# Performance work log

Hardware: AMD Instinct MI355X
Metric: run time of the kernel (lower is better)

## Reference

```python
import jax, jax.numpy as jnp
import numpy as np

N, H, R, E = 100000, 128, 30, 600000
EPS = 1e-5  # BatchNorm1d default eps


def _rgcn_layer(h, src, dst, etype, W, root, bias):
    """PyG RGCNConv: out = h @ root + bias + sum_r scatter_mean_r(h[src] @ W[r]).
    Mean is per (dst, relation) edge count."""
    n = h.shape[0]
    r_count = W.shape[0]
    seg = dst * r_count + etype                      # combined (dst, rel) segment id
    deg = jax.ops.segment_sum(jnp.ones_like(etype, dtype=h.dtype), seg,
                              num_segments=n * r_count)
    norm = 1.0 / jnp.maximum(deg[seg], 1.0)          # (E,) per-edge mean weight

    def body(out, inp):
        Wr, r = inp
        xr = h @ Wr                                  # (N,H) relation-transformed feats
        contrib = jnp.where((etype == r)[:, None], xr[src] * norm[:, None], 0.0)
        return out + jax.ops.segment_sum(contrib, dst, num_segments=n), None

    out0 = h @ root + bias
    out, _ = jax.lax.scan(body, out0, (W, jnp.arange(r_count)))
    return out


def _bn_relu(h, gamma, beta):
    # BatchNorm1d in training mode: biased batch statistics over the node dim
    mu = h.mean(axis=0)
    var = h.var(axis=0)
    return jax.nn.relu((h - mu) * jax.lax.rsqrt(var + EPS) * gamma + beta)


def setup_inputs() -> dict:
    key = jax.random.key(0)
    ks = jax.random.split(key, 16)
    s = 1.0 / np.sqrt(H)
    return {
        "x": jnp.arange(N, dtype=jnp.int32),
        "edge_index": jax.random.randint(ks[0], (2, E), 0, N, dtype=jnp.int32),
        "edge_type": jax.random.randint(ks[1], (E,), 0, R, dtype=jnp.int32),
        "emb": jax.random.normal(ks[2], (N, H), jnp.float32) * s,
        "W1": jax.random.normal(ks[3], (R, H, H), jnp.float32) * s,
        "root1": jax.random.normal(ks[4], (H, H), jnp.float32) * s,
        "b1": jnp.zeros((H,), jnp.float32),
        "g1": jnp.ones((H,), jnp.float32),
        "be1": jnp.zeros((H,), jnp.float32),
        "W2": jax.random.normal(ks[5], (R, H, H), jnp.float32) * s,
        "root2": jax.random.normal(ks[6], (H, H), jnp.float32) * s,
        "b2": jnp.zeros((H,), jnp.float32),
        "g2": jnp.ones((H,), jnp.float32),
        "be2": jnp.zeros((H,), jnp.float32),
    }


def reference(x, edge_index, edge_type, emb, W1, root1, b1, g1, be1,
              W2, root2, b2, g2, be2):
    src, dst = edge_index[0], edge_index[1]
    h = emb[x]                                        # (N,H) embedding lookup
    h = _bn_relu(_rgcn_layer(h, src, dst, edge_type, W1, root1, b1), g1, be1)
    h = _bn_relu(_rgcn_layer(h, src, dst, edge_type, W2, root2, b2), g2, be2)
    return h  # dropout is identity (deterministic reference)
```

## Files before the change

kernel.cpp:

```cpp
#include <hip/hip_runtime.h>
#include <hip/hip_bf16.h>

#define NN 100000
#define HH 128
#define RR 30
#define NE 600000
#define TILE 64
#define CH 64
#define EPAD (NE + RR * TILE)
#define NCHMAX (EPAD / TILE)
#define NB_PS ((NN + 255) / 256)
#define NBLK_BN 784
#define RPB_BN 128
#define BN_EPS 1e-5f

typedef __bf16 v8bf __attribute__((ext_vector_type(8)));
typedef float  v4f  __attribute__((ext_vector_type(4)));
typedef unsigned int v4u __attribute__((ext_vector_type(4)));

static __device__ __forceinline__ unsigned short f2b(float f) {
    unsigned int u = __float_as_uint(f);
    unsigned int r = (u + 0x7FFF + ((u >> 16) & 1)) >> 16;
    return (unsigned short)r;
}

__global__ void k_hist(const int* __restrict__ dst, const int* __restrict__ et,
                       int* __restrict__ deg, int* __restrict__ cnt) {
    __shared__ int lh[RR];
    int t = threadIdx.x;
    if (t < RR) lh[t] = 0;
    __syncthreads();
    int i = blockIdx.x * blockDim.x + t;
    if (i < NE) {
        int d = dst[i], r = et[i];
        atomicAdd(&deg[d * RR + r], 1);
        atomicAdd(&lh[r], 1);
    }
    __syncthreads();
    if (t < RR && lh[t]) atomicAdd(&cnt[t], lh[t]);
}

__global__ void k_degsum(const int* __restrict__ deg, int* __restrict__ cnt_d) {
    int d = blockIdx.x * blockDim.x + threadIdx.x;
    if (d >= NN) return;
    int s = 0;
#pragma unroll
    for (int r = 0; r < RR; ++r) s += deg[(size_t)d * RR + r];
    cnt_d[d] = s;
}

__global__ void k_scan(const int* __restrict__ cnt, int* __restrict__ cursor,
                       int* __restrict__ totals,
                       int* __restrict__ src_s, int* __restrict__ dst_s,
                       float* __restrict__ norm_s, int* __restrict__ dpos_s,
                       int* __restrict__ chunk_rel, int need_dst) {
    __shared__ int off[RR + 1];
    if (threadIdx.x == 0) {
        int acc = 0;
        for (int r = 0; r < RR; ++r) {
            off[r] = acc;
            acc += (cnt[r] + TILE - 1) / TILE;
        }
        off[RR] = acc;
        totals[0] = acc * TILE;
    }
    __syncthreads();
    for (int r = 0; r < RR; ++r) {
        for (int c = off[r] + (int)threadIdx.x; c < off[r + 1]; c += blockDim.x)
            chunk_rel[c] = r;
        int begin = off[r] * TILE + cnt[r];
        int end   = off[r + 1] * TILE;
        for (int p = begin + (int)threadIdx.x; p < end; p += blockDim.x) {
            src_s[p] = 0; norm_s[p] = 0.f;
            dpos_s[p] = NE;
            if (need_dst) dst_s[p] = 0;
        }
    }
    if (threadIdx.x == 0)
        for (int r = 0; r < RR; ++r) cursor[r] = off[r] * TILE;
}

__global__ void k_psum1(const int* __restrict__ c, int* __restrict__ bsum) {
    __shared__ int sh[256];
    int i = blockIdx.x * 256 + threadIdx.x;
    sh[threadIdx.x] = (i < NN) ? c[i] : 0;
    __syncthreads();
    for (int s = 128; s > 0; s >>= 1) {
        if (threadIdx.x < s) sh[threadIdx.x] += sh[threadIdx.x + s];
        __syncthreads();
    }
    if (threadIdx.x == 0) bsum[blockIdx.x] = sh[0];
}

__global__ void k_psum2(int* __restrict__ bsum) {
    __shared__ int sh[512];
    int t = threadIdx.x;
    sh[t] = (t < NB_PS) ? bsum[t] : 0;
    __syncthreads();
    if (t == 0) {
        int acc = 0;
        for (int b = 0; b < NB_PS; ++b) { int v = sh[b]; sh[b] = acc; acc += v; }
    }
    __syncthreads();
    if (t < NB_PS) bsum[t] = sh[t];
}

__global__ void k_psum3(const int* __restrict__ c, const int* __restrict__ bscan,
                        int* __restrict__ off, int* __restrict__ cur) {
    __shared__ int sh[256];
    int t = threadIdx.x;
    int i = blockIdx.x * 256 + t;
    int v = (i < NN) ? c[i] : 0;
    sh[t] = v;
    __syncthreads();
    for (int s = 1; s < 256; s <<= 1) {
        int a = (t >= s) ? sh[t - s] : 0;
        __syncthreads();
        sh[t] += a;
        __syncthreads();
    }
    int excl = sh[t] - v + bscan[blockIdx.x];
    if (i < NN) { off[i] = excl; cur[i] = excl; }
    if (i == 0) off[NN] = NE;
}

__global__ void k_fillds2(const int* __restrict__ off, int* __restrict__ ds2) {
    int d = blockIdx.x * blockDim.x + threadIdx.x;
    if (d >= NN) return;
    int s = off[d], e = off[d + 1];
    for (int p = s; p < e; ++p) ds2[p] = d;
}

__global__ void k_scatter(const int* __restrict__ src, const int* __restrict__ dst,
                          const int* __restrict__ et, const int* __restrict__ deg,
                          int* __restrict__ cursor, int* __restrict__ cursor_dst,
                          int* __restrict__ src_s, int* __restrict__ dst_s,
                          float* __restrict__ norm_s, int* __restrict__ dpos_s,
                          int need_dst) {
    __shared__ int lh[RR];
    __shared__ int lbase[RR];
    int t = threadIdx.x;
    if (t < RR) lh[t] = 0;
    __syncthreads();
    int i = blockIdx.x * blockDim.x + t;
    int r = 0, d = 0, lrank = 0;
    bool valid = (i < NE);
    if (valid) {
        r = et[i]; d = dst[i];
        lrank = atomicAdd(&lh[r], 1);
    }
    __syncthreads();
    if (t < RR && lh[t]) lbase[t] = atomicAdd(&cursor[t], lh[t]);
    __syncthreads();
    if (valid) {
        int pos = lbase[r] + lrank;
        src_s[pos] = src[i];
        if (need_dst) dst_s[pos] = d;
        int dg = deg[d * RR + r];
        norm_s[pos] = 1.0f / (float)(dg > 1 ? dg : 1);
        dpos_s[pos] = atomicAdd(&cursor_dst[d], 1);
    }
}

__global__ void k_convW(const float* __restrict__ W, unsigned short* __restrict__ Wt,
                        int total) {
    int idx = blockIdx.x * blockDim.x + threadIdx.x;
    if (idx >= total) return;
    int m = idx / (HH * HH);
    int rem = idx % (HH * HH);
    int k = rem / HH, c = rem % HH;
    Wt[m * HH * HH + c * HH + k] = f2b(W[idx]);
}

__global__ void k_embed(const int* __restrict__ x, const float* __restrict__ emb,
                        unsigned short* __restrict__ hb) {
    int idx = blockIdx.x * blockDim.x + threadIdx.x;
    if (idx >= NN * HH) return;
    int i = idx / HH, j = idx % HH;
    hb[idx] = f2b(emb[x[i] * HH + j]);
}

__global__ __launch_bounds__(256) void k_rootgemm(const unsigned short* __restrict__ hb,
                                                  const unsigned short* __restrict__ rootT,
                                                  const float* __restrict__ bias,
                                                  float* __restrict__ tmp) {
    __shared__ __align__(16) unsigned short Xs[TILE][HH + 8];
    __shared__ __align__(16) unsigned short Ws[HH][HH + 8];
    int base = blockIdx.x * TILE;
    int t = threadIdx.x;

    {
        int l = t >> 2, lr = t & 3;
        int row = base + l;
        for (int i = 0; i < 4; ++i) {
            int g = lr + 4 * i;
            uint4 v = {0u, 0u, 0u, 0u};
            if (row < NN) v = *reinterpret_cast<const uint4*>(hb + (size_t)row * HH + g * 8);
            *reinterpret_cast<uint4*>(&Xs[l][g * 8]) = v;
        }
    }
    for (int i = 0; i < 8; ++i) {
        int idx = t + 256 * i;
        int row = idx >> 4, g = idx & 15;
        *reinterpret_cast<uint4*>(&Ws[row][g * 8]) =
            *reinterpret_cast<const uint4*>(rootT + row * HH + g * 8);
    }
    __syncthreads();

    int w = t >> 6, lane = t & 63;
    int lr16 = lane & 15, kg = lane >> 4;
    v4f acc[8];
    for (int n = 0; n < 8; ++n) acc[n] = (v4f){0.f, 0.f, 0.f, 0.f};
#pragma unroll
    for (int kk = 0; kk < 4; ++kk) {
        int k0 = kk * 32 + kg * 8;
        v8bf a = *reinterpret_cast<const v8bf*>(&Xs[w * 16 + lr16][k0]);
#pragma unroll
        for (int n = 0; n < 8; ++n) {
            v8bf b = *reinterpret_cast<const v8bf*>(&Ws[n * 16 + lr16][k0]);
            acc[n] = __builtin_amdgcn_mfma_f32_16x16x32_bf16(a, b, acc[n], 0, 0, 0);
        }
    }
#pragma unroll
    for (int n = 0; n < 8; ++n)
        for (int j = 0; j < 4; ++j) {
            int row = base + w * 16 + kg * 4 + j;
            int col = n * 16 + lr16;
            if (row < NN) tmp[(size_t)row * HH + col] = acc[n][j] + bias[col];
        }
}

__global__ __launch_bounds__(256) void k_edgegemm_x(const unsigned short* __restrict__ hb,
                                                    const unsigned short* __restrict__ Wt,
                                                    const int* __restrict__ src_s,
                                                    const int* __restrict__ chunk_rel,
                                                    const float* __restrict__ norm_s,
                                                    const int* __restrict__ dpos_s,
                                                    const int* __restrict__ totals,
                                                    unsigned short* __restrict__ xe) {
    int ebase = blockIdx.x * TILE;
    if (ebase >= totals[0]) return;
    __shared__ __align__(16) unsigned short Ws[HH][HH + 8];
    __shared__ __align__(16) unsigned short Xs[TILE][HH];
    int t = threadIdx.x;
    int rel = chunk_rel[blockIdx.x];

    const unsigned short* Wr = Wt + (size_t)rel * HH * HH;
    for (int i = 0; i < 8; ++i) {
        int idx = t + 256 * i;
        int row = idx >> 4, g = idx & 15;
        *reinterpret_cast<uint4*>(&Ws[row][g * 8]) =
            *reinterpret_cast<const uint4*>(Wr + row * HH + g * 8);
    }

    int w = t >> 6, lane = t & 63;
    int lr16 = lane & 15, kg = lane >> 4;
    int slot = w * 16 + lr16;
    int srow = src_s[ebase + slot];
    float nrm = norm_s[ebase + slot];

    v8bf xf[4];
    const unsigned short* hrow = hb + (size_t)srow * HH + kg * 8;
#pragma unroll
    for (int kk = 0; kk < 4; ++kk)
        xf[kk] = *reinterpret_cast<const v8bf*>(hrow + kk * 32);

    __syncthreads();

    int c = slot & 7;
#pragma unroll
    for (int n = 0; n < 8; ++n) {
        v4f acc = {0.f, 0.f, 0.f, 0.f};
#pragma unroll
        for (int kk = 0; kk < 4; ++kk) {
            v8bf wf = *reinterpret_cast<const v8bf*>(&Ws[n * 16 + lr16][kk * 32 + kg * 8]);
            acc = __builtin_amdgcn_mfma_f32_16x16x32_bf16(wf, xf[kk], acc, 0, 0, 0);
        }
        unsigned long long p =
            (unsigned long long)f2b(acc[0] * nrm)
          | ((unsigned long long)f2b(acc[1] * nrm) << 16)
          | ((unsigned long long)f2b(acc[2] * nrm) << 32)
          | ((unsigned long long)f2b(acc[3] * nrm) << 48);
        int a = n * 4 + kg;
        int sw = (((a >> 1) ^ c) << 1) | (a & 1);
        *reinterpret_cast<unsigned long long*>(&Xs[slot][sw * 4]) = p;
    }
    __syncthreads();
    {
        int l = t >> 2, lr = t & 3;
        size_t drow = (size_t)dpos_s[ebase + l];
        int cs = l & 7;
        unsigned short* orow = xe + drow * HH;
#pragma unroll
        for (int i = 0; i < 4; ++i) {
            int j = lr + 4 * i;
            v4u v = *reinterpret_cast<const v4u*>(&Xs[l][(j ^ cs) * 8]);
            __builtin_nontemporal_store(v, reinterpret_cast<v4u*>(orow + j * 8));
        }
    }
}

__global__ __launch_bounds__(256) void k_edgegemm_at(const unsigned short* __restrict__ hb,
                                                     const unsigned short* __restrict__ Wt,
                                                     const int* __restrict__ src_s,
                                                     const int* __restrict__ dst_s,
                                                     const int* __restrict__ chunk_rel,
                                                     const float* __restrict__ norm_s,
                                                     const int* __restrict__ totals,
                                                     float* __restrict__ tmp) {
    int ebase = blockIdx.x * TILE;
    if (ebase >= totals[0]) return;
    __shared__ __align__(16) unsigned short Xs[TILE][HH + 8];
    __shared__ __align__(16) unsigned short Ws[HH][HH + 8];
    __shared__ int   src_l[TILE];
    __shared__ int   dst_l[TILE];
    __shared__ float nrm_l[TILE];
    int t = threadIdx.x;
    if (t < TILE) {
        src_l[t] = src_s[ebase + t];
        dst_l[t] = dst_s[ebase + t];
        nrm_l[t] = norm_s[ebase + t];
    }
    int rel = chunk_rel[blockIdx.x];
    __syncthreads();
    {
        int l = t >> 2, lr = t & 3;
        int srow = src_l[l];
        for (int i = 0; i < 4; ++i) {
            int g = lr + 4 * i;
            *reinterpret_cast<uint4*>(&Xs[l][g * 8]) =
                *reinterpret_cast<const uint4*>(hb + (size_t)srow * HH + g * 8);
        }
    }
    const unsigned short* Wr = Wt + (size_t)rel * HH * HH;
    for (int i = 0; i < 8; ++i) {
        int idx = t + 256 * i;
        int row = idx >> 4, g = idx & 15;
        *reinterpret_cast<uint4*>(&Ws[row][g * 8]) =
            *reinterpret_cast<const uint4*>(Wr + row * HH + g * 8);
    }
    __syncthreads();
    int w = t >> 6, lane = t & 63;
    int lr16 = lane & 15, kg = lane >> 4;
    v4f acc[8];
    for (int n = 0; n < 8; ++n) acc[n] = (v4f){0.f, 0.f, 0.f, 0.f};
#pragma unroll
    for (int kk = 0; kk < 4; ++kk) {
        int k0 = kk * 32 + kg * 8;
        v8bf a = *reinterpret_cast<const v8bf*>(&Xs[w * 16 + lr16][k0]);
#pragma unroll
        for (int n = 0; n < 8; ++n) {
            v8bf b = *reinterpret_cast<const v8bf*>(&Ws[n * 16 + lr16][k0]);
            acc[n] = __builtin_amdgcn_mfma_f32_16x16x32_bf16(a, b, acc[n], 0, 0, 0);
        }
    }
#pragma unroll
    for (int n = 0; n < 8; ++n)
        for (int j = 0; j < 4; ++j) {
            int slot = w * 16 + kg * 4 + j;
            int col  = n * 16 + lr16;
            atomicAdd(&tmp[(size_t)dst_l[slot] * HH + col], acc[n][j] * nrm_l[slot]);
        }
}

__global__ __launch_bounds__(256) void k_aggseg(const unsigned int* __restrict__ xe32,
                                                const int* __restrict__ ds2,
                                                float* __restrict__ tmp) {
    int wid = (blockIdx.x * blockDim.x + threadIdx.x) >> 6;
    int lane = threadIdx.x & 63;
    if (wid >= NE / CH) return;
    int c0 = wid * CH;

    int dme = ds2[c0 + lane];
    int dpre = __shfl_up(dme, 1);
    if (lane == 0) dpre = (c0 == 0) ? -1 : ds2[c0 - 1];
    unsigned long long bmask = __ballot(dme != dpre);
    int dnext = (c0 + CH < NE) ? ds2[c0 + CH] : -1;

    int dcur = __shfl(dme, 0);
    bool fresh = (bmask & 1ull) != 0;
    float a0 = 0.f, a1 = 0.f;
    for (int q0 = 0; q0 < CH; q0 += 16) {
        unsigned int v[16];
#pragma unroll
        for (int j = 0; j < 16; ++j)
            v[j] = __builtin_nontemporal_load(&xe32[(size_t)(c0 + q0 + j) * 64 + lane]);
#pragma unroll
        for (int j = 0; j < 16; ++j) {
            int q = q0 + j;
            if (q && ((bmask >> q) & 1ull)) {
                float* base = tmp + (size_t)dcur * HH + lane * 2;
                if (fresh) {
                    float2* b2 = reinterpret_cast<float2*>(base);
                    float2 o = *b2; o.x += a0; o.y += a1; *b2 = o;
                } else {
                    atomicAdd(base, a0);
                    atomicAdd(base + 1, a1);
                }
                a0 = 0.f; a1 = 0.f;
                dcur = __shfl(dme, q);
                fresh = true;
            }
            a0 += __uint_as_float(v[j] << 16);
            a1 += __uint_as_float(v[j] & 0xffff0000u);
        }
    }
    {
        bool endclean = (dnext != dcur);
        float* base = tmp + (size_t)dcur * HH + lane * 2;
        if (fresh && endclean) {
            float2* b2 = reinterpret_cast<float2*>(base);
            float2 o = *b2; o.x += a0; o.y += a1; *b2 = o;
        } else {
            atomicAdd(base, a0);
            atomicAdd(base + 1, a1);
        }
    }
}

__global__ __launch_bounds__(256) void k_bnsum1(const float* __restrict__ tmp,
                                                float* __restrict__ psum,
                                                float* __restrict__ psq) {
    int t = threadIdx.x;
    int rg = t >> 5, lane = t & 31;
    int base = blockIdx.x * RPB_BN;
    v4f s = {0.f, 0.f, 0.f, 0.f}, q = {0.f, 0.f, 0.f, 0.f};
#pragma unroll 4
    for (int i = 0; i < RPB_BN / 8; ++i) {
        int row = base + rg + 8 * i;
        if (row < NN) {
            v4f v = *reinterpret_cast<const v4f*>(tmp + (size_t)row * HH + lane * 4);
            s += v; q += v * v;
        }
    }
    __shared__ v4f shs[8][32], shq[8][32];
    shs[rg][lane] = s; shq[rg][lane] = q;
    __syncthreads();
    if (rg == 0) {
        v4f ts = shs[0][lane], tq = shq[0][lane];
#pragma unroll
        for (int k = 1; k < 8; ++k) { ts += shs[k][lane]; tq += shq[k][lane]; }
        int b = blockIdx.x;
#pragma unroll
        for (int j = 0; j < 4; ++j) {
            psum[(size_t)(lane * 4 + j) * NBLK_BN + b] = ts[j];
            psq [(size_t)(lane * 4 + j) * NBLK_BN + b] = tq[j];
        }
    }
}

__global__ void k_bnsum2(const float* __restrict__ psum, const float* __restrict__ psq,
                         const float* __restrict__ g, const float* __restrict__ be,
                         float* __restrict__ sc_g, float* __restrict__ shf_g) {
    __shared__ float ssum[HH], ssq[HH];
    int t = threadIdx.x;
    int col = t & 127;
    const float* row = ((t < 128) ? psum : psq) + (size_t)col * NBLK_BN;
    v4f a = {0.f, 0.f, 0.f, 0.f};
    for (int i = 0; i < NBLK_BN / 4; ++i)
        a += *reinterpret_cast<const v4f*>(row + i * 4);
    float acc = a[0] + a[1] + a[2] + a[3];
    if (t < 128) ssum[col] = acc; else ssq[col] = acc;
    __syncthreads();
    if (t < 128) {
        float inv_n = 1.0f / (float)NN;
        float mean = ssum[col] * inv_n;
        float var = ssq[col] * inv_n - mean * mean;
        float sc = g[col] * rsqrtf(var + BN_EPS);
        sc_g[col] = sc;
        shf_g[col] = be[col] - mean * sc;
    }
}

__global__ void k_bnapply(const float* __restrict__ tmp, const float* __restrict__ sc_g,
                          const float* __restrict__ shf_g,
                          unsigned short* __restrict__ hout,
                          float* __restrict__ fout, int write_bf16) {
    int idx = blockIdx.x * blockDim.x + threadIdx.x;
    if (idx >= NN * HH / 4) return;
    int c4 = (idx & 31) * 4;
    v4f v  = *reinterpret_cast<const v4f*>(tmp + (size_t)idx * 4);
    v4f sc = *reinterpret_cast<const v4f*>(sc_g + c4);
    v4f sh = *reinterpret_cast<const v4f*>(shf_g + c4);
    v4f r;
#pragma unroll
    for (int j = 0; j < 4; ++j) r[j] = fmaxf(v[j] * sc[j] + sh[j], 0.f);
    if (write_bf16) {
        uint2 u;
        u.x = (unsigned int)f2b(r[0]) | ((unsigned int)f2b(r[1]) << 16);
        u.y = (unsigned int)f2b(r[2]) | ((unsigned int)f2b(r[3]) << 16);
        *reinterpret_cast<uint2*>(hout + (size_t)idx * 4) = u;
    } else {
        *reinterpret_cast<v4f*>(fout + (size_t)idx * 4) = r;
    }
}

constexpr size_t OFF_DEG  = 0;
constexpr size_t OFF_HB   = OFF_DEG + (size_t)NN * RR * 4;
constexpr size_t OFF_TMP  = OFF_HB + (size_t)NN * HH * 2;
constexpr size_t OFF_W1T  = OFF_TMP + (size_t)NN * HH * 4;
constexpr size_t OFF_W2T  = OFF_W1T + (size_t)RR * HH * HH * 2;
constexpr size_t OFF_R1T  = OFF_W2T + (size_t)RR * HH * HH * 2;
constexpr size_t OFF_R2T  = OFF_R1T + (size_t)HH * HH * 2;
constexpr size_t OFF_SRCS = OFF_R2T + (size_t)HH * HH * 2;
constexpr size_t OFF_DSTS = OFF_SRCS + (size_t)EPAD * 4;
constexpr size_t OFF_NRMS = OFF_DSTS + (size_t)EPAD * 4;
constexpr size_t OFF_DPOS = OFF_NRMS + (size_t)EPAD * 4;
constexpr size_t OFF_DS2  = OFF_DPOS + (size_t)EPAD * 4;
constexpr size_t OFF_CREL = OFF_DS2 + (size_t)EPAD * 4;
constexpr size_t OFF_CNTD = OFF_CREL + ((size_t)NCHMAX * 4 + 255 & ~(size_t)255);
constexpr size_t OFF_OFFD = OFF_CNTD + ((size_t)(NN + 1) * 4 + 255 & ~(size_t)255);
constexpr size_t OFF_CURD = OFF_OFFD + ((size_t)(NN + 1) * 4 + 255 & ~(size_t)255);
constexpr size_t OFF_BSUM = OFF_CURD + ((size_t)NN * 4 + 255 & ~(size_t)255);
constexpr size_t OFF_CTRL = OFF_BSUM + ((size_t)NB_PS * 4 + 255 & ~(size_t)255);
constexpr size_t OFF_SC   = OFF_CTRL + 512;
constexpr size_t OFF_SHF  = OFF_SC + 512;
constexpr size_t OFF_PSUM = OFF_SHF + 512;
constexpr size_t OFF_PSQ  = OFF_PSUM + (size_t)HH * NBLK_BN * 4;
constexpr size_t OFF_XE   = (OFF_PSQ + (size_t)HH * NBLK_BN * 4 + 255) & ~(size_t)255;
constexpr size_t WS_MIN   = OFF_XE;
constexpr size_t WS_FULL  = OFF_XE + (size_t)EPAD * HH * 2;

extern "C" void kernel_launch(void* const* d_in, const int* in_sizes, int n_in,
                              void* d_out, int out_size, void* d_ws, size_t ws_size,
                              hipStream_t stream) {
    const int*   x     = (const int*)d_in[0];
    const int*   eidx  = (const int*)d_in[1];
    const int*   et    = (const int*)d_in[2];
    const float* emb   = (const float*)d_in[3];
    const float* W1    = (const float*)d_in[4];
    const float* root1 = (const float*)d_in[5];
    const float* b1    = (const float*)d_in[6];
    const float* g1    = (const float*)d_in[7];
    const float* be1   = (const float*)d_in[8];
    const float* W2    = (const float*)d_in[9];
    const float* root2 = (const float*)d_in[10];
    const float* b2    = (const float*)d_in[11];
    const float* g2    = (const float*)d_in[12];
    const float* be2   = (const float*)d_in[13];
    float* out = (float*)d_out;

    if (ws_size < WS_MIN) return;
    const bool full = (ws_size >= WS_FULL);
    const int need_dst = full ? 0 : 1;

    char* ws = (char*)d_ws;
    int*   deg    = (int*)(ws + OFF_DEG);
    unsigned short* hb = (unsigned short*)(ws + OFF_HB);
    float* tmp    = (float*)(ws + OFF_TMP);
    unsigned short* W1t = (unsigned short*)(ws + OFF_W1T);
    unsigned short* W2t = (unsigned short*)(ws + OFF_W2T);
    unsigned short* r1t = (unsigned short*)(ws + OFF_R1T);
    unsigned short* r2t = (unsigned short*)(ws + OFF_R2T);
    int*   src_s  = (int*)(ws + OFF_SRCS);
    int*   dst_s  = (int*)(ws + OFF_DSTS);
    float* norm_s = (float*)(ws + OFF_NRMS);
    int*   dpos_s = (int*)(ws + OFF_DPOS);
    int*   ds2    = (int*)(ws + OFF_DS2);
    int*   crel   = (int*)(ws + OFF_CREL);
    int*   cnt_d  = (int*)(ws + OFF_CNTD);
    int*   off_d  = (int*)(ws + OFF_OFFD);
    int*   cur_d  = (int*)(ws + OFF_CURD);
    int*   bsum   = (int*)(ws + OFF_BSUM);
    int*   cnt    = (int*)(ws + OFF_CTRL);
    int*   cursor = cnt + 32;
    int*   totals = cnt + 64;
    float* sc_g   = (float*)(ws + OFF_SC);
    float* shf_g  = (float*)(ws + OFF_SHF);
    float* psum   = (float*)(ws + OFF_PSUM);
    float* psq    = (float*)(ws + OFF_PSQ);
    unsigned short* xe = (unsigned short*)(ws + OFF_XE);

    const int* srcp = eidx;
    const int* dstp = eidx + NE;

    hipMemsetAsync(deg, 0, (size_t)NN * RR * 4, stream);
    hipMemsetAsync(cnt, 0, 512, stream);

    k_hist<<<(NE + 255) / 256, 256, 0, stream>>>(dstp, et, deg, cnt);
    k_degsum<<<(NN + 255) / 256, 256, 0, stream>>>(deg, cnt_d);
    k_scan<<<1, 256, 0, stream>>>(cnt, cursor, totals, src_s, dst_s, norm_s,
                                  dpos_s, crel, need_dst);
    k_psum1<<<NB_PS, 256, 0, stream>>>(cnt_d, bsum);
    k_psum2<<<1, 512, 0, stream>>>(bsum);
    k_psum3<<<NB_PS, 256, 0, stream>>>(cnt_d, bsum, off_d, cur_d);
    k_fillds2<<<(NN + 255) / 256, 256, 0, stream>>>(off_d, ds2);
    k_scatter<<<(NE + 255) / 256, 256, 0, stream>>>(srcp, dstp, et, deg, cursor, cur_d,
                                                    src_s, dst_s, norm_s, dpos_s,
                                                    need_dst);
    k_convW<<<(RR * HH * HH + 255) / 256, 256, 0, stream>>>(W1, W1t, RR * HH * HH);
    k_convW<<<(RR * HH * HH + 255) / 256, 256, 0, stream>>>(W2, W2t, RR * HH * HH);
    k_convW<<<(HH * HH + 255) / 256, 256, 0, stream>>>(root1, r1t, HH * HH);
    k_convW<<<(HH * HH + 255) / 256, 256, 0, stream>>>(root2, r2t, HH * HH);
    k_embed<<<(NN * HH + 255) / 256, 256, 0, stream>>>(x, emb, hb);

    const unsigned short* Wts[2] = {W1t, W2t};
    const unsigned short* rts[2] = {r1t, r2t};
    const float* biases[2] = {b1, b2};
    const float* gs[2]     = {g1, g2};
    const float* bes[2]    = {be1, be2};

    const int nchunks = NE / CH;
    for (int layer = 0; layer < 2; ++layer) {
        k_rootgemm<<<(NN + TILE - 1) / TILE, 256, 0, stream>>>(hb, rts[layer],
                                                               biases[layer], tmp);
        if (full) {
            k_edgegemm_x<<<EPAD / TILE, 256, 0, stream>>>(hb, Wts[layer], src_s, crel,
                                                          norm_s, dpos_s, totals, xe);
            k_aggseg<<<(nchunks + 3) / 4, 256, 0, stream>>>((const unsigned int*)xe,
                                                            ds2, tmp);
        } else {
            k_edgegemm_at<<<EPAD / TILE, 256, 0, stream>>>(hb, Wts[layer], src_s, dst_s,
                                                           crel, norm_s, totals, tmp);
        }
        k_bnsum1<<<NBLK_BN, 256, 0, stream>>>(tmp, psum, psq);
        k_bnsum2<<<1, 256, 0, stream>>>(psum, psq, gs[layer], bes[layer], sc_g, shf_g);
        k_bnapply<<<(NN * HH / 4 + 255) / 256, 256, 0, stream>>>(tmp, sc_g, shf_g,
                                                                 hb, out, layer == 0);
    }
}
```

Before: 530.5 us.

## Pack degree counts into 16-bit pairs, use hardware bf16 pack, alias edge-GEMM LDS

The per-(dst, relation) degree table now holds two 16-bit counters per 32-bit word, which halves the memset and the atomic and read traffic in the histogram, degree-sum and scatter kernels. Software bf16 rounding is replaced by the v_cvt_pk_bf16_f32 instruction in the embedding, edge GEMM and BN output paths, and the embedding kernel writes two values per thread. The edge GEMM now computes all MFMA accumulators first and then reuses the weight LDS buffer for the output staging tile, cutting shared memory per block to raise occupancy at the cost of more accumulator registers and an extra barrier. Packed counters assume no single (dst, relation) pair exceeds 65535 edges.

```diff
diff --git a/kernel.cpp b/kernel.cpp
--- a/kernel.cpp
+++ b/kernel.cpp
@@ -4,6 +4,7 @@
 #define NN 100000
 #define HH 128
 #define RR 30
+#define RR2 15
 #define NE 600000
 #define TILE 64
 #define CH 64
@@ -24,8 +25,14 @@
     return (unsigned short)r;
 }
 
+static __device__ __forceinline__ unsigned int pk_bf16(float lo, float hi) {
+    unsigned int r;
+    asm("v_cvt_pk_bf16_f32 %0, %1, %2" : "=v"(r) : "v"(lo), "v"(hi));
+    return r;
+}
+
 __global__ void k_hist(const int* __restrict__ dst, const int* __restrict__ et,
-                       int* __restrict__ deg, int* __restrict__ cnt) {
+                       unsigned int* __restrict__ deg16, int* __restrict__ cnt) {
     __shared__ int lh[RR];
     int t = threadIdx.x;
     if (t < RR) lh[t] = 0;
@@ -33,19 +40,23 @@
     int i = blockIdx.x * blockDim.x + t;
     if (i < NE) {
         int d = dst[i], r = et[i];
-        atomicAdd(&deg[d * RR + r], 1);
+        atomicAdd(&deg16[(size_t)d * RR2 + (r >> 1)], 1u << ((r & 1) * 16));
         atomicAdd(&lh[r], 1);
     }
     __syncthreads();
     if (t < RR && lh[t]) atomicAdd(&cnt[t], lh[t]);
 }
 
-__global__ void k_degsum(const int* __restrict__ deg, int* __restrict__ cnt_d) {
+__global__ void k_degsum(const unsigned int* __restrict__ deg16,
+                         int* __restrict__ cnt_d) {
     int d = blockIdx.x * blockDim.x + threadIdx.x;
     if (d >= NN) return;
     int s = 0;
 #pragma unroll
-    for (int r = 0; r < RR; ++r) s += deg[(size_t)d * RR + r];
+    for (int r2 = 0; r2 < RR2; ++r2) {
+        unsigned int v = deg16[(size_t)d * RR2 + r2];
+        s += (int)(v & 0xffffu) + (int)(v >> 16);
+    }
     cnt_d[d] = s;
 }
 
@@ -132,7 +143,8 @@
 }
 
 __global__ void k_scatter(const int* __restrict__ src, const int* __restrict__ dst,
-                          const int* __restrict__ et, const int* __restrict__ deg,
+                          const int* __restrict__ et,
+                          const unsigned int* __restrict__ deg16,
                           int* __restrict__ cursor, int* __restrict__ cursor_dst,
                           int* __restrict__ src_s, int* __restrict__ dst_s,
                           float* __restrict__ norm_s, int* __restrict__ dpos_s,
@@ -156,7 +168,7 @@
         int pos = lbase[r] + lrank;
         src_s[pos] = src[i];
         if (need_dst) dst_s[pos] = d;
-        int dg = deg[d * RR + r];
+        int dg = (int)((deg16[(size_t)d * RR2 + (r >> 1)] >> ((r & 1) * 16)) & 0xffffu);
         norm_s[pos] = 1.0f / (float)(dg > 1 ? dg : 1);
         dpos_s[pos] = atomicAdd(&cursor_dst[d], 1);
     }
@@ -173,11 +185,13 @@
 }
 
 __global__ void k_embed(const int* __restrict__ x, const float* __restrict__ emb,
-                        unsigned short* __restrict__ hb) {
+                        unsigned int* __restrict__ hb2) {
     int idx = blockIdx.x * blockDim.x + threadIdx.x;
-    if (idx >= NN * HH) return;
-    int i = idx / HH, j = idx % HH;
-    hb[idx] = f2b(emb[x[i] * HH + j]);
+    if (idx >= NN * HH / 2) return;
+    int i = idx >> 6;
+    int j2 = (idx & 63) * 2;
+    const float* p = emb + (size_t)x[i] * HH + j2;
+    hb2[idx] = pk_bf16(p[0], p[1]);
 }
 
 __global__ __launch_bounds__(256) void k_rootgemm(const unsigned short* __restrict__ hb,
@@ -240,8 +254,7 @@
                                                     unsigned short* __restrict__ xe) {
     int ebase = blockIdx.x * TILE;
     if (ebase >= totals[0]) return;
-    __shared__ __align__(16) unsigned short Ws[HH][HH + 8];
-    __shared__ __align__(16) unsigned short Xs[TILE][HH];
+    __shared__ __align__(16) unsigned short S[HH * (HH + 8)];
     int t = threadIdx.x;
     int rel = chunk_rel[blockIdx.x];
 
@@ -249,7 +262,7 @@
     for (int i = 0; i < 8; ++i) {
         int idx = t + 256 * i;
         int row = idx >> 4, g = idx & 15;
-        *reinterpret_cast<uint4*>(&Ws[row][g * 8]) =
+        *reinterpret_cast<uint4*>(&S[row * (HH + 8) + g * 8]) =
             *reinterpret_cast<const uint4*>(Wr + row * HH + g * 8);
     }
 
@@ -267,23 +280,29 @@
 
     __syncthreads();
 
+    v4f acc[8];
+#pragma unroll
+    for (int n = 0; n < 8; ++n) acc[n] = (v4f){0.f, 0.f, 0.f, 0.f};
+#pragma unroll
+    for (int n = 0; n < 8; ++n)
+#pragma unroll
+        for (int kk = 0; kk < 4; ++kk) {
+            v8bf wf = *reinterpret_cast<const v8bf*>(
+                &S[(n * 16 + lr16) * (HH + 8) + kk * 32 + kg * 8]);
+            acc[n] = __builtin_amdgcn_mfma_f32_16x16x32_bf16(wf, xf[kk], acc[n], 0, 0, 0);
+        }
+
+    __syncthreads();
+
     int c = slot & 7;
 #pragma unroll
     for (int n = 0; n < 8; ++n) {
-        v4f acc = {0.f, 0.f, 0.f, 0.f};
-#pragma unroll
-        for (int kk = 0; kk < 4; ++kk) {
-            v8bf wf = *reinterpret_cast<const v8bf*>(&Ws[n * 16 + lr16][kk * 32 + kg * 8]);
-            acc = __builtin_amdgcn_mfma_f32_16x16x32_bf16(wf, xf[kk], acc, 0, 0, 0);
-        }
-        unsigned long long p =
-            (unsigned long long)f2b(acc[0] * nrm)
-          | ((unsigned long long)f2b(acc[1] * nrm) << 16)
-          | ((unsigned long long)f2b(acc[2] * nrm) << 32)
-          | ((unsigned long long)f2b(acc[3] * nrm) << 48);
+        unsigned int w0 = pk_bf16(acc[n][0] * nrm, acc[n][1] * nrm);
+        unsigned int w1 = pk_bf16(acc[n][2] * nrm, acc[n][3] * nrm);
+        unsigned long long p = (unsigned long long)w0 | ((unsigned long long)w1 << 32);
         int a = n * 4 + kg;
         int sw = (((a >> 1) ^ c) << 1) | (a & 1);
-        *reinterpret_cast<unsigned long long*>(&Xs[slot][sw * 4]) = p;
+        *reinterpret_cast<unsigned long long*>(&S[slot * HH + sw * 4]) = p;
     }
     __syncthreads();
     {
@@ -294,7 +313,7 @@
 #pragma unroll
         for (int i = 0; i < 4; ++i) {
             int j = lr + 4 * i;
-            v4u v = *reinterpret_cast<const v4u*>(&Xs[l][(j ^ cs) * 8]);
+            v4u v = *reinterpret_cast<const v4u*>(&S[l * HH + (j ^ cs) * 8]);
             __builtin_nontemporal_store(v, reinterpret_cast<v4u*>(orow + j * 8));
         }
     }
@@ -487,8 +506,8 @@
     for (int j = 0; j < 4; ++j) r[j] = fmaxf(v[j] * sc[j] + sh[j], 0.f);
     if (write_bf16) {
         uint2 u;
-        u.x = (unsigned int)f2b(r[0]) | ((unsigned int)f2b(r[1]) << 16);
-        u.y = (unsigned int)f2b(r[2]) | ((unsigned int)f2b(r[3]) << 16);
+        u.x = pk_bf16(r[0], r[1]);
+        u.y = pk_bf16(r[2], r[3]);
         *reinterpret_cast<uint2*>(hout + (size_t)idx * 4) = u;
     } else {
         *reinterpret_cast<v4f*>(fout + (size_t)idx * 4) = r;
@@ -496,7 +515,7 @@
 }
 
 constexpr size_t OFF_DEG  = 0;
-constexpr size_t OFF_HB   = OFF_DEG + (size_t)NN * RR * 4;
+constexpr size_t OFF_HB   = OFF_DEG + (size_t)NN * RR2 * 4;
 constexpr size_t OFF_TMP  = OFF_HB + (size_t)NN * HH * 2;
 constexpr size_t OFF_W1T  = OFF_TMP + (size_t)NN * HH * 4;
 constexpr size_t OFF_W2T  = OFF_W1T + (size_t)RR * HH * HH * 2;
@@ -545,7 +564,7 @@
     const int need_dst = full ? 0 : 1;
 
     char* ws = (char*)d_ws;
-    int*   deg    = (int*)(ws + OFF_DEG);
+    unsigned int* deg16 = (unsigned int*)(ws + OFF_DEG);
     unsigned short* hb = (unsigned short*)(ws + OFF_HB);
     float* tmp    = (float*)(ws + OFF_TMP);
     unsigned short* W1t = (unsigned short*)(ws + OFF_W1T);
@@ -574,25 +593,25 @@
     const int* srcp = eidx;
     const int* dstp = eidx + NE;
 
-    hipMemsetAsync(deg, 0, (size_t)NN * RR * 4, stream);
+    hipMemsetAsync(deg16, 0, (size_t)NN * RR2 * 4, stream);
     hipMemsetAsync(cnt, 0, 512, stream);
 
-    k_hist<<<(NE + 255) / 256, 256, 0, stream>>>(dstp, et, deg, cnt);
-    k_degsum<<<(NN + 255) / 256, 256, 0, stream>>>(deg, cnt_d);
+    k_hist<<<(NE + 255) / 256, 256, 0, stream>>>(dstp, et, deg16, cnt);
+    k_degsum<<<(NN + 255) / 256, 256, 0, stream>>>(deg16, cnt_d);
     k_scan<<<1, 256, 0, stream>>>(cnt, cursor, totals, src_s, dst_s, norm_s,
                                   dpos_s, crel, need_dst);
     k_psum1<<<NB_PS, 256, 0, stream>>>(cnt_d, bsum);
     k_psum2<<<1, 512, 0, stream>>>(bsum);
     k_psum3<<<NB_PS, 256, 0, stream>>>(cnt_d, bsum, off_d, cur_d);
     k_fillds2<<<(NN + 255) / 256, 256, 0, stream>>>(off_d, ds2);
-    k_scatter<<<(NE + 255) / 256, 256, 0, stream>>>(srcp, dstp, et, deg, cursor, cur_d,
+    k_scatter<<<(NE + 255) / 256, 256, 0, stream>>>(srcp, dstp, et, deg16, cursor, cur_d,
                                                     src_s, dst_s, norm_s, dpos_s,
                                                     need_dst);
     k_convW<<<(RR * HH * HH + 255) / 256, 256, 0, stream>>>(W1, W1t, RR * HH * HH);
     k_convW<<<(RR * HH * HH + 255) / 256, 256, 0, stream>>>(W2, W2t, RR * HH * HH);
     k_convW<<<(HH * HH + 255) / 256, 256, 0, stream>>>(root1, r1t, HH * HH);
     k_convW<<<(HH * HH + 255) / 256, 256, 0, stream>>>(root2, r2t, HH * HH);
-    k_embed<<<(NN * HH + 255) / 256, 256, 0, stream>>>(x, emb, hb);
+    k_embed<<<(NN * HH / 2 + 255) / 256, 256, 0, stream>>>(x, emb, (unsigned int*)hb);
 
     const unsigned short* Wts[2] = {W1t, W2t};
     const unsigned short* rts[2] = {r1t, r2t};
```

Result: faster. 514.9 us (-2.9%).
